# Kernel tuning notes

Measured on AMD Instinct MI355X. Metric: run time of the kernel, lower is better.

## Reference

```python
import jax, jax.numpy as jnp
import numpy as np

D_MODEL = 1024
N_HEADS = 16


def setup_inputs() -> dict:
    key = jax.random.key(0)
    ks = jax.random.split(key, 5)
    B, T, C = 4, 2048, D_MODEL
    x = jax.random.normal(ks[0], (B, T, C), dtype=jnp.float32)
    W_attn = jax.random.normal(ks[1], (C, 3 * C), dtype=jnp.float32) * (1.0 / np.sqrt(C))
    b_attn = jnp.zeros((3 * C,), dtype=jnp.float32)
    W_proj = jax.random.normal(ks[2], (C, C), dtype=jnp.float32) * (1.0 / np.sqrt(C))
    b_proj = jnp.zeros((C,), dtype=jnp.float32)
    return {"x": x, "W_attn": W_attn, "b_attn": b_attn, "W_proj": W_proj, "b_proj": b_proj}


def reference(x, W_attn, b_attn, W_proj, b_proj):
    B, T, C = x.shape
    H = N_HEADS
    hd = C // H
    qkv = x @ W_attn + b_attn                      # [B,T,3C]
    q, k, v = jnp.split(qkv, 3, axis=2)
    # [B,T,C] -> [B,H,T,hd]
    q = q.reshape(B, T, H, hd).transpose(0, 2, 1, 3)
    k = k.reshape(B, T, H, hd).transpose(0, 2, 1, 3)
    v = v.reshape(B, T, H, hd).transpose(0, 2, 1, 3)
    scale = 1.0 / jnp.sqrt(jnp.float32(hd))
    attn = jnp.einsum('bhqd,bhkd->bhqk', q, k) * scale
    causal = jnp.tril(jnp.ones((T, T), dtype=bool))
    attn = jnp.where(causal[None, None], attn, -jnp.inf)
    w = jax.nn.softmax(attn, axis=-1)
    ctx = jnp.einsum('bhqk,bhkd->bhqd', w, v)      # [B,H,T,hd]
    ctx = ctx.transpose(0, 2, 1, 3).reshape(B, T, C)
    return ctx @ W_proj + b_proj
```

## Files before the change

### kernel.cpp

```cpp
#include <hip/hip_runtime.h>
#include <hip/hip_bf16.h>

typedef __bf16 bf16x8 __attribute__((ext_vector_type(8)));
typedef __bf16 bf16x4 __attribute__((ext_vector_type(4)));
typedef float f32x4 __attribute__((ext_vector_type(4)));

#define MFMA(A, B, C) __builtin_amdgcn_mfma_f32_16x16x32_bf16((A), (B), (C), 0, 0, 0)

#if __has_builtin(__builtin_amdgcn_exp2f)
#define EXP2(x) __builtin_amdgcn_exp2f(x)
#else
#define EXP2(x) exp2f(x)
#endif

#define T_SEQ 2048
#define BATCH 4
#define CDIM  1024
#define HEADS 16
#define HD    64
#define MROWS (BATCH * T_SEQ)
#define QK_SCALE 0.18033688011112042f

__device__ __forceinline__ void async_ld16(const __bf16* g, __bf16* l) {
    __builtin_amdgcn_global_load_lds(
        (const __attribute__((address_space(1))) void*)g,
        (__attribute__((address_space(3))) void*)l, 16, 0, 0);
}

__global__ __launch_bounds__(256) void conv_transpose(const float* __restrict__ src,
                                                      __bf16* __restrict__ dst,
                                                      int R, int C)
{
    __shared__ float tile[32][33];
    int c0 = blockIdx.x * 32, r0 = blockIdx.y * 32;
    int tx = threadIdx.x, ty = threadIdx.y;
#pragma unroll
    for (int i = 0; i < 4; i++)
        tile[ty + i * 8][tx] = src[(long)(r0 + ty + i * 8) * C + c0 + tx];
    __syncthreads();
#pragma unroll
    for (int i = 0; i < 4; i++)
        dst[(long)(c0 + ty + i * 8) * R + r0 + tx] = (__bf16)tile[tx][ty + i * 8];
}

__global__ __launch_bounds__(256) void conv_bf16(const float* __restrict__ src,
                                                 __bf16* __restrict__ dst)
{
    long i = ((long)blockIdx.x * 256 + threadIdx.x) * 8;
    f32x4 f0 = ((const f32x4*)(src + i))[0];
    f32x4 f1 = ((const f32x4*)(src + i))[1];
    bf16x8 v;
#pragma unroll
    for (int j = 0; j < 4; j++) { v[j] = (__bf16)f0[j]; v[4 + j] = (__bf16)f1[j]; }
    *(bf16x8*)(dst + i) = v;
}

__global__ __launch_bounds__(256) void vtrans(const __bf16* __restrict__ qkv,
                                              __bf16* __restrict__ vt)
{
    __shared__ __bf16 tile[32][33];
    int bh = blockIdx.z;
    int b = bh >> 4, h = bh & 15;
    int t0 = blockIdx.x * 32, d0 = blockIdx.y * 32;
    int tx = threadIdx.x, ty = threadIdx.y;
#pragma unroll
    for (int i = 0; i < 4; i++)
        tile[ty + i * 8][tx] =
            qkv[(long)(b * T_SEQ + t0 + ty + i * 8) * (3 * CDIM) + 2 * CDIM + h * HD + d0 + tx];
    __syncthreads();
#pragma unroll
    for (int i = 0; i < 4; i++)
        vt[(long)(bh * HD + d0 + ty + i * 8) * T_SEQ + t0 + tx] = tile[tx][ty + i * 8];
}

template <bool OUT_F32>
__global__ __launch_bounds__(256) void gemm_bt_lds(const __bf16* __restrict__ A,
                                                   const __bf16* __restrict__ Bt,
                                                   const float* __restrict__ bias,
                                                   void* __restrict__ Cv,
                                                   int M, int N, int K, int lda,
                                                   int scale_cols)
{
    __shared__ __attribute__((aligned(16))) __bf16 As[128 * 32];
    __shared__ __attribute__((aligned(16))) __bf16 Bs[128 * 32];

    const int m0 = blockIdx.y * 128, n0 = blockIdx.x * 128;
    const int t = threadIdx.x;
    const int wave = t >> 6, lane = t & 63;
    const int quad = lane >> 4, l15 = lane & 15;
    const int wm = (wave >> 1) * 64, wn = (wave & 1) * 64;

    const int srow = t >> 2;
    const int sg = t & 3;

    f32x4 acc[4][4] = {};

    for (int k0 = 0; k0 < K; k0 += 32) {
#pragma unroll
        for (int r = 0; r < 2; r++)
            async_ld16(A + (long)(m0 + r * 64 + srow) * lda + k0 + sg * 8,
                       &As[r * 2048 + t * 8]);
#pragma unroll
        for (int r = 0; r < 2; r++)
            async_ld16(Bt + (long)(n0 + r * 64 + srow) * K + k0 + sg * 8,
                       &Bs[r * 2048 + t * 8]);

        __syncthreads();

        bf16x8 af[4], bfr[4];
#pragma unroll
        for (int i = 0; i < 4; i++)
            af[i] = *(const bf16x8*)&As[(wm + i * 16 + l15) * 32 + quad * 8];
#pragma unroll
        for (int i = 0; i < 4; i++)
            bfr[i] = *(const bf16x8*)&Bs[(wn + i * 16 + l15) * 32 + quad * 8];
#pragma unroll
        for (int mi = 0; mi < 4; mi++)
#pragma unroll
            for (int ni = 0; ni < 4; ni++)
                acc[mi][ni] = MFMA(af[mi], bfr[ni], acc[mi][ni]);
        __syncthreads();
    }

    const float sc = (n0 < scale_cols) ? QK_SCALE : 1.0f;
#pragma unroll
    for (int mi = 0; mi < 4; mi++) {
#pragma unroll
        for (int ni = 0; ni < 4; ni++) {
            int col = n0 + wn + ni * 16 + l15;
            float bv = bias[col];
#pragma unroll
            for (int r = 0; r < 4; r++) {
                int row = m0 + wm + mi * 16 + quad * 4 + r;
                float v = (acc[mi][ni][r] + bv) * sc;
                if constexpr (OUT_F32)
                    ((float*)Cv)[(long)row * N + col] = v;
                else
                    ((__bf16*)Cv)[(long)row * N + col] = (__bf16)v;
            }
        }
    }
}

__global__ __launch_bounds__(256) void attn_kernel(__bf16* qkv,
                                                   const __bf16* __restrict__ vt)
{
    __shared__ __attribute__((aligned(16))) __bf16 Ks[2][64 * 32];
    __shared__ __attribute__((aligned(16))) __bf16 Vts[2][64 * 32];
    __shared__ __attribute__((aligned(16))) __bf16 Ps[8][16 * 72];

    const int bh = blockIdx.x;
    const int b = bh >> 4, h = bh & 15;
    const int qt = (int)gridDim.y - 1 - (int)blockIdx.y;
    const int q0 = qt * 128;
    const int t = threadIdx.x;
    const int wave = t >> 6, lane = t & 63;
    const int quad = lane >> 4, l15 = lane & 15;

    bf16x8 qfr[2][2];
#pragma unroll
    for (int f = 0; f < 2; f++) {
        const __bf16* qb = qkv + (long)(b * T_SEQ + q0 + f * 64 + wave * 16 + l15) * (3 * CDIM) + h * HD;
        qfr[f][0] = *(const bf16x8*)(qb + quad * 8);
        qfr[f][1] = *(const bf16x8*)(qb + 32 + quad * 8);
    }

    bf16x8 vone;
#pragma unroll
    for (int j = 0; j < 8; j++) vone[j] = (__bf16)1.0f;

    f32x4 Oacc[2][4] = {};
    f32x4 lacc[2] = {};

    const __bf16* kbase = qkv + (long)(b * T_SEQ + (t >> 2)) * (3 * CDIM)
                          + CDIM + h * HD + (t & 3) * 8;
    const __bf16* vbase = vt + ((long)bh * HD + (t >> 2)) * T_SEQ + (t & 3) * 8;

    const int ntiles = (q0 + 128) / 64;
    for (int kt = 0; kt < ntiles; kt++) {
        const __bf16* kp = kbase + (long)kt * 64 * (3 * CDIM);
        async_ld16(kp,      &Ks[0][t * 8]);
        async_ld16(kp + 32, &Ks[1][t * 8]);
        const __bf16* vp = vbase + kt * 64;
        async_ld16(vp,      &Vts[0][t * 8]);
        async_ld16(vp + 32, &Vts[1][t * 8]);
        __syncthreads();

#pragma unroll
        for (int c = 0; c < 4; c++) {
            bf16x8 kf0 = *(const bf16x8*)&Ks[0][(c * 16 + l15) * 32 + quad * 8];
            bf16x8 kf1 = *(const bf16x8*)&Ks[1][(c * 16 + l15) * 32 + quad * 8];
#pragma unroll
            for (int f = 0; f < 2; f++) {
                f32x4 z = {};
                z = MFMA(kf0, qfr[f][0], z);
                z = MFMA(kf1, qfr[f][1], z);
                const int qbf = q0 + f * 64 + wave * 16;
                const int qg = qbf + l15;
                const int kvb = kt * 64 + c * 16 + quad * 4;
                bf16x4 pk;
                if (kt * 64 + 63 > qbf) {
#pragma unroll
                    for (int r = 0; r < 4; r++) {
                        float v = (kvb + r > qg) ? -1e30f : z[r];
                        pk[r] = (__bf16)EXP2(v);
                    }
                } else {
#pragma unroll
                    for (int r = 0; r < 4; r++)
                        pk[r] = (__bf16)EXP2(z[r]);
                }
                *(bf16x4*)&Ps[wave * 2 + f][l15 * 72 + c * 16 + quad * 4] = pk;
            }
        }

        __threadfence_block();

        bf16x8 pf[2][2];
#pragma unroll
        for (int f = 0; f < 2; f++) {
            pf[f][0] = *(const bf16x8*)&Ps[wave * 2 + f][l15 * 72 + quad * 8];
            pf[f][1] = *(const bf16x8*)&Ps[wave * 2 + f][l15 * 72 + 32 + quad * 8];
            lacc[f] = MFMA(pf[f][0], vone, lacc[f]);
            lacc[f] = MFMA(pf[f][1], vone, lacc[f]);
        }
#pragma unroll
        for (int n = 0; n < 4; n++) {
            bf16x8 vf0 = *(const bf16x8*)&Vts[0][(n * 16 + l15) * 32 + quad * 8];
            bf16x8 vf1 = *(const bf16x8*)&Vts[1][(n * 16 + l15) * 32 + quad * 8];
#pragma unroll
            for (int f = 0; f < 2; f++) {
                Oacc[f][n] = MFMA(pf[f][0], vf0, Oacc[f][n]);
                Oacc[f][n] = MFMA(pf[f][1], vf1, Oacc[f][n]);
            }
        }
        __syncthreads();
    }

#pragma unroll
    for (int f = 0; f < 2; f++)
#pragma unroll
        for (int n = 0; n < 4; n++) {
            int col = h * HD + n * 16 + l15;
#pragma unroll
            for (int r = 0; r < 4; r++) {
                int row = q0 + f * 64 + wave * 16 + quad * 4 + r;
                float val = Oacc[f][n][r] / lacc[f][r];
                qkv[(long)(b * T_SEQ + row) * (3 * CDIM) + col] = (__bf16)val;
            }
        }
}

extern "C" void kernel_launch(void* const* d_in, const int* in_sizes, int n_in,
                              void* d_out, int out_size, void* d_ws, size_t ws_size,
                              hipStream_t stream) {
    (void)in_sizes; (void)n_in; (void)out_size; (void)ws_size;
    const float* x  = (const float*)d_in[0];
    const float* Wa = (const float*)d_in[1];
    const float* ba = (const float*)d_in[2];
    const float* Wp = (const float*)d_in[3];
    const float* bp = (const float*)d_in[4];
    float* out = (float*)d_out;

    char* ws = (char*)d_ws;
    __bf16* qkv = (__bf16*)(ws);
    __bf16* Wat = (__bf16*)(ws + 50331648);
    __bf16* vt  = (__bf16*)(ws + 50331648);
    __bf16* Wpt = (__bf16*)(ws + 50331648);
    __bf16* xbf = (__bf16*)d_out;

    conv_bf16<<<dim3(MROWS * CDIM / (256 * 8)), 256, 0, stream>>>(x, xbf);
    conv_transpose<<<dim3(3 * CDIM / 32, CDIM / 32), dim3(32, 8), 0, stream>>>(Wa, Wat, CDIM, 3 * CDIM);

    gemm_bt_lds<false><<<dim3(3 * CDIM / 128, MROWS / 128), 256, 0, stream>>>(
        xbf, Wat, ba, qkv, MROWS, 3 * CDIM, CDIM, CDIM, CDIM);

    vtrans<<<dim3(T_SEQ / 32, HD / 32, BATCH * HEADS), dim3(32, 8), 0, stream>>>(qkv, vt);

    attn_kernel<<<dim3(BATCH * HEADS, T_SEQ / 128), 256, 0, stream>>>(qkv, vt);

    conv_transpose<<<dim3(CDIM / 32, CDIM / 32), dim3(32, 8), 0, stream>>>(Wp, Wpt, CDIM, CDIM);

    gemm_bt_lds<true><<<dim3(CDIM / 128, MROWS / 128), 256, 0, stream>>>(
        qkv, Wpt, bp, out, MROWS, CDIM, CDIM, 3 * CDIM, 0);
}
```

Measured before the change: 268.2 us.

## Replace GEMM with 256x256 tiled, double-buffered, 8-wave pipelined MFMA kernel

Replaces the simple 128x128 single-buffered GEMM with a 256x256-tile, 512-thread kernel. The new kernel uses double-buffered LDS with async global-to-LDS loads and an XOR-swizzled layout to avoid bank conflicts. It interleaves four MFMA phases with staged prefetches and adds workgroup-ID swizzling for L2 locality and s_setprio around compute. This is meant to hide global-load latency and raise MFMA utilization in both projection GEMMs, at the cost of 128KB of LDS per block and hand-tuned waitcnt logic that is fragile.

```diff
diff --git a/kernel.cpp b/kernel.cpp
--- a/kernel.cpp
+++ b/kernel.cpp
@@ -20,6 +20,7 @@
 #define HD    64
 #define MROWS (BATCH * T_SEQ)
 #define QK_SCALE 0.18033688011112042f
+#define KTILES (CDIM / 64)
 
 __device__ __forceinline__ void async_ld16(const __bf16* g, __bf16* l) {
     __builtin_amdgcn_global_load_lds(
@@ -73,66 +74,157 @@
         vt[(long)(bh * HD + d0 + ty + i * 8) * T_SEQ + t0 + tx] = tile[tx][ty + i * 8];
 }
 
+#define STAGE_A(buf, kt, s)                                                      \
+    do {                                                                         \
+        async_ld16(Asrc + (long)((s) * 64) * lda + (kt) * 64,                    \
+                   &lds[buf][0][(s) * 4096 + sdst]);                             \
+        async_ld16(Asrc + (long)((s) * 64 + 128) * lda + (kt) * 64,              \
+                   &lds[buf][0][(s) * 4096 + 8192 + sdst]);                      \
+    } while (0)
+
+#define STAGE_B(buf, kt, s)                                                      \
+    do {                                                                         \
+        async_ld16(Bsrc + (long)((s) * 128) * CDIM + (kt) * 64,                  \
+                   &lds[buf][1][(s) * 8192 + sdst]);                             \
+        async_ld16(Bsrc + (long)((s) * 128 + 64) * CDIM + (kt) * 64,             \
+                   &lds[buf][1][(s) * 8192 + 4096 + sdst]);                      \
+    } while (0)
+
 template <bool OUT_F32>
-__global__ __launch_bounds__(256) void gemm_bt_lds(const __bf16* __restrict__ A,
-                                                   const __bf16* __restrict__ Bt,
-                                                   const float* __restrict__ bias,
-                                                   void* __restrict__ Cv,
-                                                   int M, int N, int K, int lda,
-                                                   int scale_cols)
-{
-    __shared__ __attribute__((aligned(16))) __bf16 As[128 * 32];
-    __shared__ __attribute__((aligned(16))) __bf16 Bs[128 * 32];
-
-    const int m0 = blockIdx.y * 128, n0 = blockIdx.x * 128;
+__global__ __launch_bounds__(512, 2) void gemm8p(const __bf16* __restrict__ A,
+                                                 const __bf16* __restrict__ Bt,
+                                                 const float* __restrict__ bias,
+                                                 void* __restrict__ Cv,
+                                                 int N, int lda, int scale_cols)
+{
+    __shared__ __attribute__((aligned(16))) __bf16 lds[2][2][256 * 64];
+
+    const int nwg = (int)gridDim.x;
+    const int bid = (int)blockIdx.x;
+    const int swz = (bid & 7) * (nwg >> 3) + (bid >> 3);
+    const int nbx = N >> 8;
+    const int n0 = (swz % nbx) * 256;
+    const int m0 = (swz / nbx) * 256;
+
     const int t = threadIdx.x;
     const int wave = t >> 6, lane = t & 63;
     const int quad = lane >> 4, l15 = lane & 15;
-    const int wm = (wave >> 1) * 64, wn = (wave & 1) * 64;
-
-    const int srow = t >> 2;
-    const int sg = t & 3;
-
-    f32x4 acc[4][4] = {};
-
-    for (int k0 = 0; k0 < K; k0 += 32) {
-#pragma unroll
-        for (int r = 0; r < 2; r++)
-            async_ld16(A + (long)(m0 + r * 64 + srow) * lda + k0 + sg * 8,
-                       &As[r * 2048 + t * 8]);
-#pragma unroll
-        for (int r = 0; r < 2; r++)
-            async_ld16(Bt + (long)(n0 + r * 64 + srow) * K + k0 + sg * 8,
-                       &Bs[r * 2048 + t * 8]);
-
-        __syncthreads();
-
-        bf16x8 af[4], bfr[4];
-#pragma unroll
-        for (int i = 0; i < 4; i++)
-            af[i] = *(const bf16x8*)&As[(wm + i * 16 + l15) * 32 + quad * 8];
-#pragma unroll
-        for (int i = 0; i < 4; i++)
-            bfr[i] = *(const bf16x8*)&Bs[(wn + i * 16 + l15) * 32 + quad * 8];
-#pragma unroll
-        for (int mi = 0; mi < 4; mi++)
-#pragma unroll
-            for (int ni = 0; ni < 4; ni++)
-                acc[mi][ni] = MFMA(af[mi], bfr[ni], acc[mi][ni]);
-        __syncthreads();
+    const int wm = wave >> 2;
+    const int wn = wave & 3;
+
+    const int srow = t >> 3;
+    const int scol = ((t & 7) * 8) ^ ((srow & 7) << 3);
+    const int sdst = srow * 64 + (t & 7) * 8;
+    const __bf16* Asrc = A + (long)(m0 + srow) * lda + scol;
+    const __bf16* Bsrc = Bt + (long)(n0 + srow) * CDIM + scol;
+
+    const int kx0 = (quad * 8) ^ ((l15 & 7) << 3);
+    const int kx1 = (32 + quad * 8) ^ ((l15 & 7) << 3);
+    const int arow = (wm * 128 + l15) * 64;
+    const int brow = (wn * 64 + l15) * 64;
+
+    f32x4 acc[8][4] = {};
+    bf16x8 a[4][2], bb[4][2];
+
+    STAGE_A(0, 0, 0); STAGE_B(0, 0, 0); STAGE_B(0, 0, 1); STAGE_A(0, 0, 1);
+    STAGE_A(1, 1, 0); STAGE_B(1, 1, 0); STAGE_B(1, 1, 1);
+    asm volatile("s_waitcnt vmcnt(6)" ::: "memory");
+    __builtin_amdgcn_s_barrier();
+
+    for (int kt = 0; kt < KTILES; ++kt) {
+        const int cur = kt & 1;
+        const __bf16* Ac = &lds[cur][0][0];
+        const __bf16* Bc = &lds[cur][1][0];
+
+#pragma unroll
+        for (int mf = 0; mf < 4; mf++) {
+            a[mf][0] = *(const bf16x8*)&Ac[arow + mf * 1024 + kx0];
+            a[mf][1] = *(const bf16x8*)&Ac[arow + mf * 1024 + kx1];
+        }
+#pragma unroll
+        for (int nf = 0; nf < 2; nf++) {
+            bb[nf][0] = *(const bf16x8*)&Bc[brow + nf * 1024 + kx0];
+            bb[nf][1] = *(const bf16x8*)&Bc[brow + nf * 1024 + kx1];
+        }
+        if (kt + 1 < KTILES) STAGE_A((kt + 1) & 1, kt + 1, 1);
+        __builtin_amdgcn_s_barrier();
+        asm volatile("s_waitcnt lgkmcnt(0)" ::: "memory");
+        __builtin_amdgcn_s_setprio(1);
+#pragma unroll
+        for (int mf = 0; mf < 4; mf++)
+#pragma unroll
+            for (int nf = 0; nf < 2; nf++) {
+                acc[mf][nf] = MFMA(a[mf][0], bb[nf][0], acc[mf][nf]);
+                acc[mf][nf] = MFMA(a[mf][1], bb[nf][1], acc[mf][nf]);
+            }
+        __builtin_amdgcn_s_setprio(0);
+        __builtin_amdgcn_s_barrier();
+
+#pragma unroll
+        for (int nf = 2; nf < 4; nf++) {
+            bb[nf][0] = *(const bf16x8*)&Bc[brow + nf * 1024 + kx0];
+            bb[nf][1] = *(const bf16x8*)&Bc[brow + nf * 1024 + kx1];
+        }
+        if (kt + 2 < KTILES) STAGE_A(cur, kt + 2, 0);
+        __builtin_amdgcn_s_barrier();
+        asm volatile("s_waitcnt lgkmcnt(0)" ::: "memory");
+        __builtin_amdgcn_s_setprio(1);
+#pragma unroll
+        for (int mf = 0; mf < 4; mf++)
+#pragma unroll
+            for (int nf = 2; nf < 4; nf++) {
+                acc[mf][nf] = MFMA(a[mf][0], bb[nf][0], acc[mf][nf]);
+                acc[mf][nf] = MFMA(a[mf][1], bb[nf][1], acc[mf][nf]);
+            }
+        __builtin_amdgcn_s_setprio(0);
+        __builtin_amdgcn_s_barrier();
+
+#pragma unroll
+        for (int mf = 0; mf < 4; mf++) {
+            a[mf][0] = *(const bf16x8*)&Ac[arow + 4096 + mf * 1024 + kx0];
+            a[mf][1] = *(const bf16x8*)&Ac[arow + 4096 + mf * 1024 + kx1];
+        }
+        if (kt + 2 < KTILES) STAGE_B(cur, kt + 2, 0);
+        __builtin_amdgcn_s_barrier();
+        asm volatile("s_waitcnt lgkmcnt(0)" ::: "memory");
+        __builtin_amdgcn_s_setprio(1);
+#pragma unroll
+        for (int mf = 0; mf < 4; mf++)
+#pragma unroll
+            for (int nf = 2; nf < 4; nf++) {
+                acc[4 + mf][nf] = MFMA(a[mf][0], bb[nf][0], acc[4 + mf][nf]);
+                acc[4 + mf][nf] = MFMA(a[mf][1], bb[nf][1], acc[4 + mf][nf]);
+            }
+        __builtin_amdgcn_s_setprio(0);
+        __builtin_amdgcn_s_barrier();
+
+        if (kt + 2 < KTILES) STAGE_B(cur, kt + 2, 1);
+        __builtin_amdgcn_s_barrier();
+        __builtin_amdgcn_s_setprio(1);
+#pragma unroll
+        for (int mf = 0; mf < 4; mf++)
+#pragma unroll
+            for (int nf = 0; nf < 2; nf++) {
+                acc[4 + mf][nf] = MFMA(a[mf][0], bb[nf][0], acc[4 + mf][nf]);
+                acc[4 + mf][nf] = MFMA(a[mf][1], bb[nf][1], acc[4 + mf][nf]);
+            }
+        __builtin_amdgcn_s_setprio(0);
+        if (kt < KTILES - 2) { asm volatile("s_waitcnt vmcnt(6)" ::: "memory"); }
+        else                 { asm volatile("s_waitcnt vmcnt(0)" ::: "memory"); }
+        __builtin_amdgcn_s_barrier();
     }
 
     const float sc = (n0 < scale_cols) ? QK_SCALE : 1.0f;
 #pragma unroll
-    for (int mi = 0; mi < 4; mi++) {
-#pragma unroll
-        for (int ni = 0; ni < 4; ni++) {
-            int col = n0 + wn + ni * 16 + l15;
-            float bv = bias[col];
+    for (int mf = 0; mf < 8; mf++) {
+#pragma unroll
+        for (int nf = 0; nf < 4; nf++) {
+            const int col = n0 + wn * 64 + nf * 16 + l15;
+            const float bv = bias[col];
 #pragma unroll
             for (int r = 0; r < 4; r++) {
-                int row = m0 + wm + mi * 16 + quad * 4 + r;
-                float v = (acc[mi][ni][r] + bv) * sc;
+                const int row = m0 + wm * 128 + mf * 16 + quad * 4 + r;
+                float v = (acc[mf][nf][r] + bv) * sc;
                 if constexpr (OUT_F32)
                     ((float*)Cv)[(long)row * N + col] = v;
                 else
@@ -272,8 +364,8 @@
     conv_bf16<<<dim3(MROWS * CDIM / (256 * 8)), 256, 0, stream>>>(x, xbf);
     conv_transpose<<<dim3(3 * CDIM / 32, CDIM / 32), dim3(32, 8), 0, stream>>>(Wa, Wat, CDIM, 3 * CDIM);
 
-    gemm_bt_lds<false><<<dim3(3 * CDIM / 128, MROWS / 128), 256, 0, stream>>>(
-        xbf, Wat, ba, qkv, MROWS, 3 * CDIM, CDIM, CDIM, CDIM);
+    gemm8p<false><<<dim3((MROWS / 256) * (3 * CDIM / 256)), 512, 0, stream>>>(
+        xbf, Wat, ba, qkv, 3 * CDIM, CDIM, CDIM);
 
     vtrans<<<dim3(T_SEQ / 32, HD / 32, BATCH * HEADS), dim3(32, 8), 0, stream>>>(qkv, vt);
 
@@ -281,6 +373,6 @@
 
     conv_transpose<<<dim3(CDIM / 32, CDIM / 32), dim3(32, 8), 0, stream>>>(Wp, Wpt, CDIM, CDIM);
 
-    gemm_bt_lds<true><<<dim3(CDIM / 128, MROWS / 128), 256, 0, stream>>>(
-        qkv, Wpt, bp, out, MROWS, CDIM, CDIM, 3 * CDIM, 0);
-}
+    gemm8p<true><<<dim3((MROWS / 256) * (CDIM / 256)), 512, 0, stream>>>(
+        qkv, Wpt, bp, out, CDIM, 3 * CDIM, 0);
+}
```

Result: faster. 262.4 us (-2.2%).
